# Optimization experiments

Measured on AMD Instinct MI355X. Metric: run time of the kernel, lower is better.

The kernel has to match this reference:

```python
import jax, jax.numpy as jnp
import numpy as np

SIN, TEMB, EMB, S = 128, 512, 1024, 64
BATCH, T = 4, 4096


def setup_inputs() -> dict:
    key = jax.random.key(0)
    ks = jax.random.split(key, 16)

    def w(k, *shape):
        return jax.random.normal(k, shape, jnp.float32) / np.float32(np.sqrt(shape[0]))

    return {
        "time_embed": jax.random.normal(ks[0], (SIN,), jnp.float32),
        "x": jax.random.normal(ks[1], (BATCH, T, EMB), jnp.float32),
        "W1": w(ks[2], SIN, TEMB), "b1": jnp.zeros((TEMB,), jnp.float32),
        "W2": w(ks[3], TEMB, TEMB), "b2": jnp.zeros((TEMB,), jnp.float32),
        "WA": w(ks[4], TEMB, S), "bA": jnp.zeros((S,), jnp.float32),
        "WB": w(ks[5], TEMB, S, EMB), "bB": jnp.zeros((S, EMB), jnp.float32),
        "WC": w(ks[6], TEMB, EMB, S), "bC": jnp.zeros((EMB, S), jnp.float32),
        "WD": w(ks[7], TEMB, EMB), "bD": jnp.zeros((EMB,), jnp.float32),
        "Wdl": w(ks[8], TEMB, S), "bdl": jnp.zeros((S,), jnp.float32),
        "MA": w(ks[9], SIN, S), "mA": jnp.zeros((S,), jnp.float32),
        "MB": w(ks[10], SIN, S, EMB), "mB": jnp.zeros((S, EMB), jnp.float32),
        "MC": w(ks[11], SIN, EMB, S), "mC": jnp.zeros((EMB, S), jnp.float32),
        "MD": w(ks[12], SIN, EMB), "mD": jnp.zeros((EMB,), jnp.float32),
        "Mdl": w(ks[13], SIN, S), "mdl": jnp.zeros((S,), jnp.float32),
    }


def _ssm_forward(time_embed, x, W1, b1, W2, b2, WA, bA, WB, bB, WC, bC, WD, bD,
                 Wdl, bdl, MA, mA, MB, mB, MC, mC, MD, mD, Mdl, mdl):
    # time-dependent parameter generation
    t = jax.nn.silu(time_embed @ W1 + b1)
    t = t @ W2 + b2  # [TEMB]

    A_base = -jax.nn.softplus(t @ WA + bA)                       # [S]
    B_base = jnp.einsum('t,tse->se', t, WB) + bB                 # [S,E]
    C_base = jnp.einsum('t,tes->es', t, WC) + bC                 # [E,S]
    D_base = t @ WD + bD                                         # [E]
    delta_base = jax.nn.softplus(t @ Wdl + bdl) + 1e-4           # [S]

    A = A_base * jax.nn.sigmoid(time_embed @ MA + mA)
    Bm = B_base * jax.nn.sigmoid(jnp.einsum('t,tse->se', time_embed, MB) + mB)
    C = C_base * jax.nn.sigmoid(jnp.einsum('t,tes->es', time_embed, MC) + mC)
    D = D_base * jax.nn.sigmoid(time_embed @ MD + mD)
    delta = delta_base * jax.nn.sigmoid(time_embed @ Mdl + mdl)  # [S]

    A_bar = jnp.exp(delta * A)          # [S]
    B_bar = delta[:, None] * Bm         # [S,E]

    xt = jnp.swapaxes(x, 0, 1)          # [T,B,E]

    def step(h, x_t):                   # h: [B,S], x_t: [B,E]
        h_new = A_bar * h + x_t @ B_bar.T
        y = h_new @ C.T                 # [B,E]
        return h_new, y

    h0 = jnp.zeros((x.shape[0], A_bar.shape[0]), x.dtype)
    _, ys = jax.lax.scan(step, h0, xt)  # ys: [T,B,E]
    return jnp.swapaxes(ys, 0, 1) + D * x


def reference(time_embed, x, W1, b1, W2, b2, WA, bA, WB, bB, WC, bC, WD, bD,
              Wdl, bdl, MA, mA, MB, mB, MC, mC, MD, mD, Mdl, mdl):
    return _ssm_forward(time_embed, x, W1, b1, W2, b2, WA, bA, WB, bB, WC, bC,
                        WD, bD, Wdl, bdl, MA, mA, MB, mB, MC, mC, MD, mD, Mdl, mdl)
```

## Files before the change

kernel.cpp:

```cpp
#include <hip/hip_runtime.h>
#include <math.h>

#define SIN_ 128
#define TEMB_ 512
#define EMB_ 1024
#define S_ 64
#define B_ 4
#define T_ 4096
#define NROW (B_*T_)
#define L_ 32
#define NC_ (T_/L_)

#define PSTR 132224
#define FA   132096
#define FDL  132160

#define WS_T1     0
#define WS_T2     512
#define WS_DELTA  1024
#define WS_ABAR   1088
#define WS_EL     1152
#define WS_FAC    1216
#define WS_D      3264
#define WS_BMT    4288
#define WS_CT     69824
#define WS_P      135360
#define WS_HLOC   135360
#define WS_CHEND  1183936
#define WS_CARRY  1216704

__device__ __forceinline__ float sigmoidf_(float x){ return 1.f/(1.f+expf(-x)); }
__device__ __forceinline__ float softplusf_(float x){ return x>20.f ? x : log1pf(expf(x)); }
__device__ __forceinline__ float4 sig4_(float4 g){
  float4 r; r.x=sigmoidf_(g.x); r.y=sigmoidf_(g.y); r.z=sigmoidf_(g.z); r.w=sigmoidf_(g.w); return r;
}

__device__ __forceinline__ float4 colsum64(const float4* __restrict__ W, size_t strideB,
                                           const float* __restrict__ coef){
  const char* p = (const char*)W;
  float4 b0 = *(const float4*)p;
  float4 b1 = *(const float4*)(p + strideB);
  float4 b2 = *(const float4*)(p + 2*strideB);
  float4 b3 = *(const float4*)(p + 3*strideB);
  p += 4*strideB;
  float4 acc = {0.f,0.f,0.f,0.f};
  #pragma unroll
  for (int step=0; step<16; ++step){
    float4 c0v=b0, c1v=b1, c2v=b2, c3v=b3;
    if (step < 15){
      b0 = *(const float4*)p;
      b1 = *(const float4*)(p + strideB);
      b2 = *(const float4*)(p + 2*strideB);
      b3 = *(const float4*)(p + 3*strideB);
      p += 4*strideB;
    }
    float c0 = coef[4*step+0], c1 = coef[4*step+1], c2 = coef[4*step+2], c3 = coef[4*step+3];
    acc.x = fmaf(c0,c0v.x,acc.x); acc.y = fmaf(c0,c0v.y,acc.y); acc.z = fmaf(c0,c0v.z,acc.z); acc.w = fmaf(c0,c0v.w,acc.w);
    acc.x = fmaf(c1,c1v.x,acc.x); acc.y = fmaf(c1,c1v.y,acc.y); acc.z = fmaf(c1,c1v.z,acc.z); acc.w = fmaf(c1,c1v.w,acc.w);
    acc.x = fmaf(c2,c2v.x,acc.x); acc.y = fmaf(c2,c2v.y,acc.y); acc.z = fmaf(c2,c2v.z,acc.z); acc.w = fmaf(c2,c2v.w,acc.w);
    acc.x = fmaf(c3,c3v.x,acc.x); acc.y = fmaf(c3,c3v.y,acc.y); acc.z = fmaf(c3,c3v.z,acc.z); acc.w = fmaf(c3,c3v.w,acc.w);
  }
  return acc;
}

__global__ void k_t1(const float* __restrict__ te, const float* __restrict__ W1,
                     const float* __restrict__ b1, float* __restrict__ ws){
  __shared__ float ste[SIN_];
  int tid = threadIdx.x;
  ste[tid] = te[tid]; ste[tid+64] = te[tid+64];
  __syncthreads();
  int j = blockIdx.x*64 + tid;
  float a = b1[j];
  #pragma unroll 16
  for (int i=0;i<SIN_;i++) a += ste[i]*W1[i*TEMB_ + j];
  ws[WS_T1 + j] = a * sigmoidf_(a);
}

__global__ __launch_bounds__(512) void k_t2(const float* __restrict__ W2,
                                            const float* __restrict__ b2,
                                            float* __restrict__ ws){
  __shared__ float st1[TEMB_];
  __shared__ float red[8][64];
  int tid = threadIdx.x;
  st1[tid] = ws[WS_T1 + tid];
  __syncthreads();
  int jl = tid & 63, kc = tid >> 6;
  int j = blockIdx.x*64 + jl;
  float p = 0.f;
  #pragma unroll 8
  for (int i=0;i<64;i++){
    int k = kc*64 + i;
    p += st1[k]*W2[k*TEMB_ + j];
  }
  red[kc][jl] = p;
  __syncthreads();
  if (tid < 64){
    float a = b2[blockIdx.x*64 + tid];
    #pragma unroll
    for (int c=0;c<8;c++) a += red[c][tid];
    ws[WS_T2 + blockIdx.x*64 + tid] = a;
  }
}

__global__ __launch_bounds__(256) void k_partial(
    const float* __restrict__ te,
    const float* __restrict__ WB, const float* __restrict__ MB,
    const float* __restrict__ WC, const float* __restrict__ MC,
    const float* __restrict__ WD, const float* __restrict__ MD,
    const float* __restrict__ WA, const float* __restrict__ MA,
    const float* __restrict__ Wdl, const float* __restrict__ Mdl,
    float* __restrict__ ws){
  __shared__ float st2[TEMB_];
  __shared__ float ste[SIN_];
  int tid = threadIdx.x;
  st2[tid] = ws[WS_T2 + tid];
  st2[tid+256] = ws[WS_T2 + tid + 256];
  if (tid < SIN_) ste[tid] = te[tid];
  __syncthreads();
  int bb = blockIdx.x;
  if (bb < 1280){
    int region = bb >= 640 ? 1 : 0;
    int lb = bb - region*640;
    int tile = lb/10, ch = lb - tile*10;
    int q = tile*256 + tid;
    const float4* base;
    const float* coef;
    if (ch < 8){
      base = (const float4*)(region==0 ? WB : WC) + (size_t)(ch*64)*16384 + q;
      coef = st2 + ch*64;
    } else {
      base = (const float4*)(region==0 ? MB : MC) + (size_t)((ch-8)*64)*16384 + q;
      coef = ste + (ch-8)*64;
    }
    float4 a = colsum64(base, (size_t)16384*16, coef);
    ((float4*)(ws + WS_P + ch*PSTR))[region*16384 + q] = a;
  } else if (bb < 1290){
    int ch = bb - 1280;
    const float4* base;
    const float* coef;
    if (ch < 8){
      base = (const float4*)WD + (ch*64)*256 + tid;
      coef = st2 + ch*64;
    } else {
      base = (const float4*)MD + ((ch-8)*64)*256 + tid;
      coef = ste + (ch-8)*64;
    }
    float4 a = colsum64(base, (size_t)256*16, coef);
    ((float4*)(ws + WS_P + ch*PSTR))[32768 + tid] = a;
  } else if (bb == 1290){
    int c = tid>>6, s = tid&63;
    float p = 0.f;
    #pragma unroll 8
    for (int i=0;i<128;i++) p += st2[c*128+i]*WA[(c*128+i)*64 + s];
    ws[WS_P + c*PSTR + FA + s] = p;
    if (tid < 64){
      float g = 0.f;
      #pragma unroll 8
      for (int i=0;i<128;i++) g += ste[i]*MA[i*64 + s];
      ws[WS_P + 4*PSTR + FA + s] = g;
    }
  } else {
    int c = tid>>6, s = tid&63;
    float p = 0.f;
    #pragma unroll 8
    for (int i=0;i<128;i++) p += st2[c*128+i]*Wdl[(c*128+i)*64 + s];
    ws[WS_P + c*PSTR + FDL + s] = p;
    if (tid < 64){
      float g = 0.f;
      #pragma unroll 8
      for (int i=0;i<128;i++) g += ste[i]*Mdl[i*64 + s];
      ws[WS_P + 4*PSTR + FDL + s] = g;
    }
  }
}

__global__ __launch_bounds__(256) void k_finalize(
    const float* __restrict__ bB, const float* __restrict__ mB,
    const float* __restrict__ bC, const float* __restrict__ mC,
    const float* __restrict__ bD, const float* __restrict__ mD,
    const float* __restrict__ bA_, const float* __restrict__ mA_,
    const float* __restrict__ bdl, const float* __restrict__ mdl,
    float* __restrict__ ws){
  int tid = threadIdx.x, bb = blockIdx.x;
  if (bb < 129){
    int q = (bb < 128) ? bb*256 + tid : 32768 + tid;
    float4 a = {0.f,0.f,0.f,0.f};
    #pragma unroll
    for (int c=0;c<8;c++){
      float4 v = ((const float4*)(ws + WS_P + c*PSTR))[q];
      a.x += v.x; a.y += v.y; a.z += v.z; a.w += v.w;
    }
    float4 g8 = ((const float4*)(ws + WS_P + 8*PSTR))[q];
    float4 g9 = ((const float4*)(ws + WS_P + 9*PSTR))[q];
    float4 g = make_float4(g8.x+g9.x, g8.y+g9.y, g8.z+g9.z, g8.w+g9.w);
    if (bb < 128){
      if (q < 16384){
        float4 b4 = ((const float4*)bB)[q];
        float4 m4 = ((const float4*)mB)[q];
        float4 sg = sig4_(make_float4(g.x+m4.x, g.y+m4.y, g.z+m4.z, g.w+m4.w));
        float4 v = make_float4((a.x+b4.x)*sg.x,(a.y+b4.y)*sg.y,(a.z+b4.z)*sg.z,(a.w+b4.w)*sg.w);
        int o = q*4; int s = o>>10; int e = o&1023;
        ws[WS_BMT + (e+0)*64 + s] = v.x;
        ws[WS_BMT + (e+1)*64 + s] = v.y;
        ws[WS_BMT + (e+2)*64 + s] = v.z;
        ws[WS_BMT + (e+3)*64 + s] = v.w;
      } else {
        int q2 = q - 16384;
        float4 b4 = ((const float4*)bC)[q2];
        float4 m4 = ((const float4*)mC)[q2];
        float4 sg = sig4_(make_float4(g.x+m4.x, g.y+m4.y, g.z+m4.z, g.w+m4.w));
        float4 v = make_float4((a.x+b4.x)*sg.x,(a.y+b4.y)*sg.y,(a.z+b4.z)*sg.z,(a.w+b4.w)*sg.w);
        int o = q2*4; int e = o>>6; int s = o&63;
        ws[WS_CT + (s+0)*1024 + e] = v.x;
        ws[WS_CT + (s+1)*1024 + e] = v.y;
        ws[WS_CT + (s+2)*1024 + e] = v.z;
        ws[WS_CT + (s+3)*1024 + e] = v.w;
      }
    } else {
      float4 b4 = ((const float4*)bD)[tid];
      float4 m4 = ((const float4*)mD)[tid];
      float4 sg = sig4_(make_float4(g.x+m4.x, g.y+m4.y, g.z+m4.z, g.w+m4.w));
      float4 v = make_float4((a.x+b4.x)*sg.x,(a.y+b4.y)*sg.y,(a.z+b4.z)*sg.z,(a.w+b4.w)*sg.w);
      ((float4*)(ws + WS_D))[tid] = v;
    }
  } else {
    __shared__ float sda[64];
    if (tid < 64){
      int s = tid;
      float sa = ws[WS_P+0*PSTR+FA+s]+ws[WS_P+1*PSTR+FA+s]+ws[WS_P+2*PSTR+FA+s]+ws[WS_P+3*PSTR+FA+s];
      float ga = ws[WS_P+4*PSTR+FA+s];
      float A = -softplusf_(sa + bA_[s]) * sigmoidf_(ga + mA_[s]);
      float sd = ws[WS_P+0*PSTR+FDL+s]+ws[WS_P+1*PSTR+FDL+s]+ws[WS_P+2*PSTR+FDL+s]+ws[WS_P+3*PSTR+FDL+s];
      float gd = ws[WS_P+4*PSTR+FDL+s];
      float delta = (softplusf_(sd + bdl[s]) + 1e-4f) * sigmoidf_(gd + mdl[s]);
      float da = delta * A;
      sda[s] = da;
      ws[WS_DELTA+s] = delta;
      ws[WS_ABAR+s]  = expf(da);
      ws[WS_EL+s]    = expf((float)L_*da);
    }
    __syncthreads();
    for (int idx=tid; idx<L_*S_; idx+=256){
      int tl = idx>>6, s = idx&63;
      ws[WS_FAC+idx] = expf((float)(tl+1)*sda[s]);
    }
  }
}

__global__ __launch_bounds__(256) void k_scan(const float* __restrict__ x, float* __restrict__ ws){
  __shared__ float Xs[32][68];
  __shared__ float BsT[64][68];
  __shared__ float Us[32][65];
  __shared__ float sdl[S_], sab[S_];
  int tid = threadIdx.x;
  int bb = blockIdx.x;
  int row0 = (bb>>7)*T_ + (bb&127)*L_;
  if (tid<64){ sdl[tid]=ws[WS_DELTA+tid]; sab[tid]=ws[WS_ABAR+tid]; }
  float acc[2][4];
  #pragma unroll
  for (int i=0;i<2;i++)
    #pragma unroll
    for (int j=0;j<4;j++) acc[i][j]=0.f;
  int ty = tid>>4, tx = tid&15;
  const float4* x4 = (const float4*)x;
  const float4* BmT4 = (const float4*)(ws + WS_BMT);
  for (int kk=0; kk<EMB_; kk+=64){
    #pragma unroll
    for (int t=0;t<2;t++){
      int fl = t*256+tid; int rr = fl>>4, cq = fl&15;
      float4 xv = x4[(size_t)(row0+rr)*256 + (kk>>2) + cq];
      *(float4*)&Xs[rr][cq*4] = xv;
    }
    #pragma unroll
    for (int t=0;t<4;t++){
      int fl = t*256+tid; int rr = fl>>4, cq = fl&15;
      float4 bv = BmT4[(size_t)(kk+rr)*16 + cq];
      *(float4*)&BsT[rr][cq*4] = bv;
    }
    __syncthreads();
    #pragma unroll 8
    for (int k=0;k<64;k++){
      float4 b4 = *(const float4*)&BsT[k][4*tx];
      float x0 = Xs[2*ty+0][k], x1 = Xs[2*ty+1][k];
      acc[0][0]+=x0*b4.x; acc[0][1]+=x0*b4.y; acc[0][2]+=x0*b4.z; acc[0][3]+=x0*b4.w;
      acc[1][0]+=x1*b4.x; acc[1][1]+=x1*b4.y; acc[1][2]+=x1*b4.z; acc[1][3]+=x1*b4.w;
    }
    __syncthreads();
  }
  #pragma unroll
  for (int i=0;i<2;i++)
    #pragma unroll
    for (int j=0;j<4;j++)
      Us[2*ty+i][4*tx+j] = acc[i][j]*sdl[4*tx+j];
  __syncthreads();
  if (tid<64){
    int s = tid; float h = 0.f, ab = sab[s];
    #pragma unroll 8
    for (int t=0;t<L_;t++){
      h = fmaf(ab, h, Us[t][s]);
      ws[WS_HLOC + (row0+t)*S_ + s] = h;
    }
    ws[WS_CHEND + bb*S_ + s] = h;
  }
}

__global__ void k_carry(float* __restrict__ ws){
  int tid = threadIdx.x;
  int b = tid>>6, s = tid&63;
  float el = ws[WS_EL + s];
  float carry = 0.f;
  #pragma unroll 8
  for (int c=0;c<NC_;c++){
    int idx = (b*NC_ + c)*S_ + s;
    ws[WS_CARRY + idx] = carry;
    carry = fmaf(el, carry, ws[WS_CHEND + idx]);
  }
}

__global__ __launch_bounds__(256) void k_out(const float* __restrict__ x,
                                             const float* __restrict__ ws,
                                             float* __restrict__ out){
  __shared__ float Cts[64][68];
  __shared__ float Hs[64][68];
  int tid = threadIdx.x;
  int bb = blockIdx.x;
  int rt = bb & 255, et = bb >> 8;
  int row0 = rt*64, e0 = et*64;
  int b = row0 >> 12;
  int cbase = b*NC_ + ((row0 & (T_-1)) >> 5);
  const float4* hl4 = (const float4*)(ws + WS_HLOC);
  const float4* fc4 = (const float4*)(ws + WS_FAC);
  const float4* cr4 = (const float4*)(ws + WS_CARRY);
  const float4* CT4 = (const float4*)(ws + WS_CT);
  #pragma unroll
  for (int t=0;t<4;t++){
    int fl = t*256+tid; int rr = fl>>4, q = fl&15;
    float4 h = hl4[(size_t)(row0+rr)*16 + q];
    float4 f = fc4[(rr & (L_-1))*16 + q];
    float4 c = cr4[(cbase + (rr>>5))*16 + q];
    float4 hv = make_float4(h.x+f.x*c.x, h.y+f.y*c.y, h.z+f.z*c.z, h.w+f.w*c.w);
    *(float4*)&Hs[rr][q*4] = hv;
    float4 ct = CT4[(size_t)rr*256 + (e0>>2) + q];
    *(float4*)&Cts[rr][q*4] = ct;
  }
  __syncthreads();
  int ty = tid>>4, tx = tid&15;
  float acc[4][4];
  #pragma unroll
  for (int i=0;i<4;i++)
    #pragma unroll
    for (int j=0;j<4;j++) acc[i][j]=0.f;
  #pragma unroll 8
  for (int s=0;s<64;s++){
    float4 c4 = *(const float4*)&Cts[s][4*tx];
    float h0 = Hs[4*ty+0][s], h1 = Hs[4*ty+1][s], h2 = Hs[4*ty+2][s], h3 = Hs[4*ty+3][s];
    acc[0][0]+=h0*c4.x; acc[0][1]+=h0*c4.y; acc[0][2]+=h0*c4.z; acc[0][3]+=h0*c4.w;
    acc[1][0]+=h1*c4.x; acc[1][1]+=h1*c4.y; acc[1][2]+=h1*c4.z; acc[1][3]+=h1*c4.w;
    acc[2][0]+=h2*c4.x; acc[2][1]+=h2*c4.y; acc[2][2]+=h2*c4.z; acc[2][3]+=h2*c4.w;
    acc[3][0]+=h3*c4.x; acc[3][1]+=h3*c4.y; acc[3][2]+=h3*c4.z; acc[3][3]+=h3*c4.w;
  }
  float4 d4 = ((const float4*)(ws + WS_D))[(e0>>2) + tx];
  #pragma unroll
  for (int i=0;i<4;i++){
    int row = row0 + 4*ty + i;
    float4 x4v = reinterpret_cast<const float4*>(x + (size_t)row*EMB_ + e0)[tx];
    float4 o;
    o.x = acc[i][0] + d4.x*x4v.x;
    o.y = acc[i][1] + d4.y*x4v.y;
    o.z = acc[i][2] + d4.z*x4v.z;
    o.w = acc[i][3] + d4.w*x4v.w;
    reinterpret_cast<float4*>(out + (size_t)row*EMB_ + e0)[tx] = o;
  }
}

extern "C" void kernel_launch(void* const* d_in, const int* in_sizes, int n_in,
                              void* d_out, int out_size, void* d_ws, size_t ws_size,
                              hipStream_t stream){
  const float* te  = (const float*)d_in[0];
  const float* x   = (const float*)d_in[1];
  const float* W1  = (const float*)d_in[2];
  const float* b1  = (const float*)d_in[3];
  const float* W2  = (const float*)d_in[4];
  const float* b2  = (const float*)d_in[5];
  const float* WA  = (const float*)d_in[6];
  const float* bA  = (const float*)d_in[7];
  const float* WB  = (const float*)d_in[8];
  const float* bB  = (const float*)d_in[9];
  const float* WC  = (const float*)d_in[10];
  const float* bC  = (const float*)d_in[11];
  const float* WD  = (const float*)d_in[12];
  const float* bD  = (const float*)d_in[13];
  const float* Wdl = (const float*)d_in[14];
  const float* bdl = (const float*)d_in[15];
  const float* MA  = (const float*)d_in[16];
  const float* mA  = (const float*)d_in[17];
  const float* MB  = (const float*)d_in[18];
  const float* mB  = (const float*)d_in[19];
  const float* MC  = (const float*)d_in[20];
  const float* mC  = (const float*)d_in[21];
  const float* MD  = (const float*)d_in[22];
  const float* mD  = (const float*)d_in[23];
  const float* Mdl = (const float*)d_in[24];
  const float* mdl = (const float*)d_in[25];
  float* ws  = (float*)d_ws;
  float* out = (float*)d_out;

  k_t1<<<8,64,0,stream>>>(te, W1, b1, ws);
  k_t2<<<8,512,0,stream>>>(W2, b2, ws);
  k_partial<<<1292,256,0,stream>>>(te, WB,MB, WC,MC, WD,MD, WA,MA, Wdl,Mdl, ws);
  k_finalize<<<130,256,0,stream>>>(bB,mB, bC,mC, bD,mD, bA,mA, bdl,mdl, ws);
  k_scan<<<512,256,0,stream>>>(x, ws);
  k_carry<<<1,256,0,stream>>>(ws);
  k_out<<<4096,256,0,stream>>>(x, ws, out);
}
```

Baseline: 197.5 us.

## Restructure parameter reduction into wider k-chunks with bf16 partial sums

Reorganizes the large weight-contraction kernel so each block reduces 32 rows of TEMB/SIN over four float4 columns per thread, down from 64 rows by one float4. Blocks drop from 1292 to 662, and occupancy is hinted with launch_bounds(256,2). Partial sums for B and C are now stored as bf16 to cut the workspace write and re-read traffic in the finalize kernel. This shrinks intermediate traffic but adds rounding error to the partial sums, and the finalize step now reads 16+4 partials instead of 10.

```diff
diff --git a/kernel.cpp b/kernel.cpp
--- a/kernel.cpp
+++ b/kernel.cpp
@@ -11,9 +11,10 @@
 #define L_ 32
 #define NC_ (T_/L_)
 
-#define PSTR 132224
-#define FA   132096
-#define FDL  132160
+#define GK 32
+#define NSL 16
+#define NCH 16
+#define NGCH 4
 
 #define WS_T1     0
 #define WS_T2     512
@@ -24,43 +25,30 @@
 #define WS_D      3264
 #define WS_BMT    4288
 #define WS_CT     69824
-#define WS_P      135360
-#define WS_HLOC   135360
-#define WS_CHEND  1183936
-#define WS_CARRY  1216704
+#define WS_PD     135360
+#define WS_PDG    151744
+#define WS_PA     155840
+#define WS_PDL    156160
+#define WS_PBF    156480
+#define WS_HLOC   156480
+#define WS_CHEND  1205056
+#define WS_CARRY  1237824
 
 __device__ __forceinline__ float sigmoidf_(float x){ return 1.f/(1.f+expf(-x)); }
 __device__ __forceinline__ float softplusf_(float x){ return x>20.f ? x : log1pf(expf(x)); }
 __device__ __forceinline__ float4 sig4_(float4 g){
   float4 r; r.x=sigmoidf_(g.x); r.y=sigmoidf_(g.y); r.z=sigmoidf_(g.z); r.w=sigmoidf_(g.w); return r;
 }
-
-__device__ __forceinline__ float4 colsum64(const float4* __restrict__ W, size_t strideB,
-                                           const float* __restrict__ coef){
-  const char* p = (const char*)W;
-  float4 b0 = *(const float4*)p;
-  float4 b1 = *(const float4*)(p + strideB);
-  float4 b2 = *(const float4*)(p + 2*strideB);
-  float4 b3 = *(const float4*)(p + 3*strideB);
-  p += 4*strideB;
-  float4 acc = {0.f,0.f,0.f,0.f};
-  #pragma unroll
-  for (int step=0; step<16; ++step){
-    float4 c0v=b0, c1v=b1, c2v=b2, c3v=b3;
-    if (step < 15){
-      b0 = *(const float4*)p;
-      b1 = *(const float4*)(p + strideB);
-      b2 = *(const float4*)(p + 2*strideB);
-      b3 = *(const float4*)(p + 3*strideB);
-      p += 4*strideB;
-    }
-    float c0 = coef[4*step+0], c1 = coef[4*step+1], c2 = coef[4*step+2], c3 = coef[4*step+3];
-    acc.x = fmaf(c0,c0v.x,acc.x); acc.y = fmaf(c0,c0v.y,acc.y); acc.z = fmaf(c0,c0v.z,acc.z); acc.w = fmaf(c0,c0v.w,acc.w);
-    acc.x = fmaf(c1,c1v.x,acc.x); acc.y = fmaf(c1,c1v.y,acc.y); acc.z = fmaf(c1,c1v.z,acc.z); acc.w = fmaf(c1,c1v.w,acc.w);
-    acc.x = fmaf(c2,c2v.x,acc.x); acc.y = fmaf(c2,c2v.y,acc.y); acc.z = fmaf(c2,c2v.z,acc.z); acc.w = fmaf(c2,c2v.w,acc.w);
-    acc.x = fmaf(c3,c3v.x,acc.x); acc.y = fmaf(c3,c3v.y,acc.y); acc.z = fmaf(c3,c3v.z,acc.z); acc.w = fmaf(c3,c3v.w,acc.w);
-  }
-  return acc;
+__device__ __forceinline__ unsigned short f2bf(float x){
+  unsigned int u = __float_as_uint(x);
+  unsigned int r = (u + 0x7FFFu + ((u>>16)&1u)) >> 16;
+  return (unsigned short)r;
+}
+__device__ __forceinline__ ushort4 pack4(float4 v){
+  return make_ushort4(f2bf(v.x),f2bf(v.y),f2bf(v.z),f2bf(v.w));
+}
+__device__ __forceinline__ float bf2f(unsigned short h){
+  return __uint_as_float(((unsigned int)h)<<16);
 }
 
 __global__ void k_t1(const float* __restrict__ te, const float* __restrict__ W1,
@@ -102,7 +90,7 @@
   }
 }
 
-__global__ __launch_bounds__(256) void k_partial(
+__global__ __launch_bounds__(256,2) void k_partial(
     const float* __restrict__ te,
     const float* __restrict__ WB, const float* __restrict__ MB,
     const float* __restrict__ WC, const float* __restrict__ MC,
@@ -117,59 +105,114 @@
   st2[tid+256] = ws[WS_T2 + tid + 256];
   if (tid < SIN_) ste[tid] = te[tid];
   __syncthreads();
+  unsigned short* pbf = (unsigned short*)(ws + WS_PBF);
   int bb = blockIdx.x;
-  if (bb < 1280){
-    int region = bb >= 640 ? 1 : 0;
-    int lb = bb - region*640;
-    int tile = lb/10, ch = lb - tile*10;
-    int q = tile*256 + tid;
-    const float4* base;
-    const float* coef;
-    if (ch < 8){
-      base = (const float4*)(region==0 ? WB : WC) + (size_t)(ch*64)*16384 + q;
-      coef = st2 + ch*64;
-    } else {
-      base = (const float4*)(region==0 ? MB : MC) + (size_t)((ch-8)*64)*16384 + q;
-      coef = ste + (ch-8)*64;
-    }
-    float4 a = colsum64(base, (size_t)16384*16, coef);
-    ((float4*)(ws + WS_P + ch*PSTR))[region*16384 + q] = a;
-  } else if (bb < 1290){
-    int ch = bb - 1280;
-    const float4* base;
-    const float* coef;
-    if (ch < 8){
-      base = (const float4*)WD + (ch*64)*256 + tid;
-      coef = st2 + ch*64;
-    } else {
-      base = (const float4*)MD + ((ch-8)*64)*256 + tid;
-      coef = ste + (ch-8)*64;
-    }
-    float4 a = colsum64(base, (size_t)256*16, coef);
-    ((float4*)(ws + WS_P + ch*PSTR))[32768 + tid] = a;
-  } else if (bb == 1290){
-    int c = tid>>6, s = tid&63;
-    float p = 0.f;
-    #pragma unroll 8
-    for (int i=0;i<128;i++) p += st2[c*128+i]*WA[(c*128+i)*64 + s];
-    ws[WS_P + c*PSTR + FA + s] = p;
+  if (bb < 512){
+    int r = bb>>8, rem = bb&255, j = rem>>4, c = rem&15;
+    const float4* W4 = (const float4*)(r ? WC : WB);
+    const float4* base = W4 + (size_t)(c*GK)*16384 + j*1024 + tid;
+    const float* coef = st2 + c*GK;
+    float4 a0={0,0,0,0}, a1={0,0,0,0}, a2={0,0,0,0}, a3={0,0,0,0};
+    #pragma unroll 4
+    for (int k=0;k<GK;k++){
+      const float4* p = base + (size_t)k*16384;
+      float4 w0=p[0], w1=p[256], w2=p[512], w3=p[768];
+      float cv = coef[k];
+      a0.x=fmaf(cv,w0.x,a0.x); a0.y=fmaf(cv,w0.y,a0.y); a0.z=fmaf(cv,w0.z,a0.z); a0.w=fmaf(cv,w0.w,a0.w);
+      a1.x=fmaf(cv,w1.x,a1.x); a1.y=fmaf(cv,w1.y,a1.y); a1.z=fmaf(cv,w1.z,a1.z); a1.w=fmaf(cv,w1.w,a1.w);
+      a2.x=fmaf(cv,w2.x,a2.x); a2.y=fmaf(cv,w2.y,a2.y); a2.z=fmaf(cv,w2.z,a2.z); a2.w=fmaf(cv,w2.w,a2.w);
+      a3.x=fmaf(cv,w3.x,a3.x); a3.y=fmaf(cv,w3.y,a3.y); a3.z=fmaf(cv,w3.z,a3.z); a3.w=fmaf(cv,w3.w,a3.w);
+    }
+    ushort4* dst = (ushort4*)pbf + (size_t)((r*NSL+j)*NCH + c)*1024;
+    dst[tid]     = pack4(a0);
+    dst[tid+256] = pack4(a1);
+    dst[tid+512] = pack4(a2);
+    dst[tid+768] = pack4(a3);
+  } else if (bb < 640){
+    int g = bb-512, r = g>>6, rem = g&63, j = rem>>2, cg = rem&3;
+    const float4* M4 = (const float4*)(r ? MC : MB);
+    const float4* base = M4 + (size_t)(cg*GK)*16384 + j*1024 + tid;
+    const float* coef = ste + cg*GK;
+    float4 a0={0,0,0,0}, a1={0,0,0,0}, a2={0,0,0,0}, a3={0,0,0,0};
+    #pragma unroll 4
+    for (int k=0;k<GK;k++){
+      const float4* p = base + (size_t)k*16384;
+      float4 w0=p[0], w1=p[256], w2=p[512], w3=p[768];
+      float cv = coef[k];
+      a0.x=fmaf(cv,w0.x,a0.x); a0.y=fmaf(cv,w0.y,a0.y); a0.z=fmaf(cv,w0.z,a0.z); a0.w=fmaf(cv,w0.w,a0.w);
+      a1.x=fmaf(cv,w1.x,a1.x); a1.y=fmaf(cv,w1.y,a1.y); a1.z=fmaf(cv,w1.z,a1.z); a1.w=fmaf(cv,w1.w,a1.w);
+      a2.x=fmaf(cv,w2.x,a2.x); a2.y=fmaf(cv,w2.y,a2.y); a2.z=fmaf(cv,w2.z,a2.z); a2.w=fmaf(cv,w2.w,a2.w);
+      a3.x=fmaf(cv,w3.x,a3.x); a3.y=fmaf(cv,w3.y,a3.y); a3.z=fmaf(cv,w3.z,a3.z); a3.w=fmaf(cv,w3.w,a3.w);
+    }
+    ushort4* dst = (ushort4*)pbf + (size_t)(2097152/4) + (size_t)((r*NSL+j)*NGCH + cg)*1024;
+    dst[tid]     = pack4(a0);
+    dst[tid+256] = pack4(a1);
+    dst[tid+512] = pack4(a2);
+    dst[tid+768] = pack4(a3);
+  } else if (bb < 656){
+    int c = bb-640;
+    const float4* base = (const float4*)WD + (size_t)(c*GK)*256 + tid;
+    const float* coef = st2 + c*GK;
+    float4 a={0,0,0,0};
+    #pragma unroll 4
+    for (int k=0;k<GK;k++){
+      float4 w = base[(size_t)k*256];
+      float cv = coef[k];
+      a.x=fmaf(cv,w.x,a.x); a.y=fmaf(cv,w.y,a.y); a.z=fmaf(cv,w.z,a.z); a.w=fmaf(cv,w.w,a.w);
+    }
+    ((float4*)(ws + WS_PD))[c*256 + tid] = a;
+  } else if (bb < 660){
+    int cg = bb-656;
+    const float4* base = (const float4*)MD + (size_t)(cg*GK)*256 + tid;
+    const float* coef = ste + cg*GK;
+    float4 a={0,0,0,0};
+    #pragma unroll 4
+    for (int k=0;k<GK;k++){
+      float4 w = base[(size_t)k*256];
+      float cv = coef[k];
+      a.x=fmaf(cv,w.x,a.x); a.y=fmaf(cv,w.y,a.y); a.z=fmaf(cv,w.z,a.z); a.w=fmaf(cv,w.w,a.w);
+    }
+    ((float4*)(ws + WS_PDG))[cg*256 + tid] = a;
+  } else {
+    const float* Wm = (bb==660) ? WA : Wdl;
+    const float* Mm = (bb==660) ? MA : Mdl;
+    int outbase = (bb==660) ? WS_PA : WS_PDL;
+    __shared__ float red[16][68];
+    int q = tid&15, kr = tid>>4;
+    float4 acc={0,0,0,0};
+    const float4* W4 = (const float4*)Wm;
+    #pragma unroll 4
+    for (int it=0; it<32; ++it){
+      int k = it*16 + kr;
+      float4 w = W4[k*16 + q];
+      float cv = st2[k];
+      acc.x=fmaf(cv,w.x,acc.x); acc.y=fmaf(cv,w.y,acc.y); acc.z=fmaf(cv,w.z,acc.z); acc.w=fmaf(cv,w.w,acc.w);
+    }
+    red[kr][4*q+0]=acc.x; red[kr][4*q+1]=acc.y; red[kr][4*q+2]=acc.z; red[kr][4*q+3]=acc.w;
+    __syncthreads();
     if (tid < 64){
-      float g = 0.f;
-      #pragma unroll 8
-      for (int i=0;i<128;i++) g += ste[i]*MA[i*64 + s];
-      ws[WS_P + 4*PSTR + FA + s] = g;
-    }
-  } else {
-    int c = tid>>6, s = tid&63;
-    float p = 0.f;
-    #pragma unroll 8
-    for (int i=0;i<128;i++) p += st2[c*128+i]*Wdl[(c*128+i)*64 + s];
-    ws[WS_P + c*PSTR + FDL + s] = p;
+      float s = 0.f;
+      #pragma unroll
+      for (int g=0;g<16;g++) s += red[g][tid];
+      ws[outbase + tid] = s;
+    }
+    __syncthreads();
+    float4 gac={0,0,0,0};
+    const float4* M4 = (const float4*)Mm;
+    #pragma unroll 4
+    for (int it=0; it<8; ++it){
+      int k = it*16 + kr;
+      float4 w = M4[k*16 + q];
+      float cv = ste[k];
+      gac.x=fmaf(cv,w.x,gac.x); gac.y=fmaf(cv,w.y,gac.y); gac.z=fmaf(cv,w.z,gac.z); gac.w=fmaf(cv,w.w,gac.w);
+    }
+    red[kr][4*q+0]=gac.x; red[kr][4*q+1]=gac.y; red[kr][4*q+2]=gac.z; red[kr][4*q+3]=gac.w;
+    __syncthreads();
     if (tid < 64){
-      float g = 0.f;
-      #pragma unroll 8
-      for (int i=0;i<128;i++) g += ste[i]*Mdl[i*64 + s];
-      ws[WS_P + 4*PSTR + FDL + s] = g;
+      float s = 0.f;
+      #pragma unroll
+      for (int g=0;g<16;g++) s += red[g][tid];
+      ws[outbase + 64 + tid] = s;
     }
   }
 }
@@ -182,57 +225,70 @@
     const float* __restrict__ bdl, const float* __restrict__ mdl,
     float* __restrict__ ws){
   int tid = threadIdx.x, bb = blockIdx.x;
-  if (bb < 129){
-    int q = (bb < 128) ? bb*256 + tid : 32768 + tid;
-    float4 a = {0.f,0.f,0.f,0.f};
-    #pragma unroll
-    for (int c=0;c<8;c++){
-      float4 v = ((const float4*)(ws + WS_P + c*PSTR))[q];
-      a.x += v.x; a.y += v.y; a.z += v.z; a.w += v.w;
-    }
-    float4 g8 = ((const float4*)(ws + WS_P + 8*PSTR))[q];
-    float4 g9 = ((const float4*)(ws + WS_P + 9*PSTR))[q];
-    float4 g = make_float4(g8.x+g9.x, g8.y+g9.y, g8.z+g9.z, g8.w+g9.w);
-    if (bb < 128){
-      if (q < 16384){
-        float4 b4 = ((const float4*)bB)[q];
-        float4 m4 = ((const float4*)mB)[q];
-        float4 sg = sig4_(make_float4(g.x+m4.x, g.y+m4.y, g.z+m4.z, g.w+m4.w));
-        float4 v = make_float4((a.x+b4.x)*sg.x,(a.y+b4.y)*sg.y,(a.z+b4.z)*sg.z,(a.w+b4.w)*sg.w);
-        int o = q*4; int s = o>>10; int e = o&1023;
-        ws[WS_BMT + (e+0)*64 + s] = v.x;
-        ws[WS_BMT + (e+1)*64 + s] = v.y;
-        ws[WS_BMT + (e+2)*64 + s] = v.z;
-        ws[WS_BMT + (e+3)*64 + s] = v.w;
-      } else {
-        int q2 = q - 16384;
-        float4 b4 = ((const float4*)bC)[q2];
-        float4 m4 = ((const float4*)mC)[q2];
-        float4 sg = sig4_(make_float4(g.x+m4.x, g.y+m4.y, g.z+m4.z, g.w+m4.w));
-        float4 v = make_float4((a.x+b4.x)*sg.x,(a.y+b4.y)*sg.y,(a.z+b4.z)*sg.z,(a.w+b4.w)*sg.w);
-        int o = q2*4; int e = o>>6; int s = o&63;
-        ws[WS_CT + (s+0)*1024 + e] = v.x;
-        ws[WS_CT + (s+1)*1024 + e] = v.y;
-        ws[WS_CT + (s+2)*1024 + e] = v.z;
-        ws[WS_CT + (s+3)*1024 + e] = v.w;
-      }
-    } else {
-      float4 b4 = ((const float4*)bD)[tid];
-      float4 m4 = ((const float4*)mD)[tid];
+  const ushort4* pbf4 = (const ushort4*)(ws + WS_PBF);
+  if (bb < 128){
+    int r = bb>>6;
+    int q = (bb&63)*256 + tid;
+    int j = q>>10, p = q&1023;
+    float4 a = {0,0,0,0};
+    size_t wbase = (size_t)((r*NSL+j)*NCH)*1024 + p;
+    #pragma unroll
+    for (int c=0;c<NCH;c++){
+      ushort4 v = pbf4[wbase + (size_t)c*1024];
+      a.x += bf2f(v.x); a.y += bf2f(v.y); a.z += bf2f(v.z); a.w += bf2f(v.w);
+    }
+    float4 g = {0,0,0,0};
+    size_t gbase = (size_t)(2097152/4) + (size_t)((r*NSL+j)*NGCH)*1024 + p;
+    #pragma unroll
+    for (int cg=0;cg<NGCH;cg++){
+      ushort4 v = pbf4[gbase + (size_t)cg*1024];
+      g.x += bf2f(v.x); g.y += bf2f(v.y); g.z += bf2f(v.z); g.w += bf2f(v.w);
+    }
+    if (r == 0){
+      float4 b4 = ((const float4*)bB)[q];
+      float4 m4 = ((const float4*)mB)[q];
       float4 sg = sig4_(make_float4(g.x+m4.x, g.y+m4.y, g.z+m4.z, g.w+m4.w));
       float4 v = make_float4((a.x+b4.x)*sg.x,(a.y+b4.y)*sg.y,(a.z+b4.z)*sg.z,(a.w+b4.w)*sg.w);
-      ((float4*)(ws + WS_D))[tid] = v;
-    }
+      int o = q*4; int s = o>>10; int e = o&1023;
+      ws[WS_BMT + (e+0)*64 + s] = v.x;
+      ws[WS_BMT + (e+1)*64 + s] = v.y;
+      ws[WS_BMT + (e+2)*64 + s] = v.z;
+      ws[WS_BMT + (e+3)*64 + s] = v.w;
+    } else {
+      float4 b4 = ((const float4*)bC)[q];
+      float4 m4 = ((const float4*)mC)[q];
+      float4 sg = sig4_(make_float4(g.x+m4.x, g.y+m4.y, g.z+m4.z, g.w+m4.w));
+      float4 v = make_float4((a.x+b4.x)*sg.x,(a.y+b4.y)*sg.y,(a.z+b4.z)*sg.z,(a.w+b4.w)*sg.w);
+      int o = q*4; int e = o>>6; int s = o&63;
+      ws[WS_CT + (s+0)*1024 + e] = v.x;
+      ws[WS_CT + (s+1)*1024 + e] = v.y;
+      ws[WS_CT + (s+2)*1024 + e] = v.z;
+      ws[WS_CT + (s+3)*1024 + e] = v.w;
+    }
+  } else if (bb == 128){
+    float4 a = {0,0,0,0};
+    #pragma unroll
+    for (int c=0;c<NCH;c++){
+      float4 v = ((const float4*)(ws + WS_PD))[c*256 + tid];
+      a.x+=v.x; a.y+=v.y; a.z+=v.z; a.w+=v.w;
+    }
+    float4 g = {0,0,0,0};
+    #pragma unroll
+    for (int cg=0;cg<NGCH;cg++){
+      float4 v = ((const float4*)(ws + WS_PDG))[cg*256 + tid];
+      g.x+=v.x; g.y+=v.y; g.z+=v.z; g.w+=v.w;
+    }
+    float4 b4 = ((const float4*)bD)[tid];
+    float4 m4 = ((const float4*)mD)[tid];
+    float4 sg = sig4_(make_float4(g.x+m4.x, g.y+m4.y, g.z+m4.z, g.w+m4.w));
+    float4 v = make_float4((a.x+b4.x)*sg.x,(a.y+b4.y)*sg.y,(a.z+b4.z)*sg.z,(a.w+b4.w)*sg.w);
+    ((float4*)(ws + WS_D))[tid] = v;
   } else {
     __shared__ float sda[64];
     if (tid < 64){
       int s = tid;
-      float sa = ws[WS_P+0*PSTR+FA+s]+ws[WS_P+1*PSTR+FA+s]+ws[WS_P+2*PSTR+FA+s]+ws[WS_P+3*PSTR+FA+s];
-      float ga = ws[WS_P+4*PSTR+FA+s];
-      float A = -softplusf_(sa + bA_[s]) * sigmoidf_(ga + mA_[s]);
-      float sd = ws[WS_P+0*PSTR+FDL+s]+ws[WS_P+1*PSTR+FDL+s]+ws[WS_P+2*PSTR+FDL+s]+ws[WS_P+3*PSTR+FDL+s];
-      float gd = ws[WS_P+4*PSTR+FDL+s];
-      float delta = (softplusf_(sd + bdl[s]) + 1e-4f) * sigmoidf_(gd + mdl[s]);
+      float A = -softplusf_(ws[WS_PA+s] + bA_[s]) * sigmoidf_(ws[WS_PA+64+s] + mA_[s]);
+      float delta = (softplusf_(ws[WS_PDL+s] + bdl[s]) + 1e-4f) * sigmoidf_(ws[WS_PDL+64+s] + mdl[s]);
       float da = delta * A;
       sda[s] = da;
       ws[WS_DELTA+s] = delta;
@@ -407,7 +463,7 @@
 
   k_t1<<<8,64,0,stream>>>(te, W1, b1, ws);
   k_t2<<<8,512,0,stream>>>(W2, b2, ws);
-  k_partial<<<1292,256,0,stream>>>(te, WB,MB, WC,MC, WD,MD, WA,MA, Wdl,Mdl, ws);
+  k_partial<<<662,256,0,stream>>>(te, WB,MB, WC,MC, WD,MD, WA,MA, Wdl,Mdl, ws);
   k_finalize<<<130,256,0,stream>>>(bB,mB, bC,mC, bD,mD, bA,mA, bdl,mdl, ws);
   k_scan<<<512,256,0,stream>>>(x, ws);
   k_carry<<<1,256,0,stream>>>(ws);
```

Measured after the change: 192.0 us. 1.03x faster.
